# Kernel optimization log

Measured on AMD Instinct MI355X. Metric: run time of the kernel, lower is better.

Reference implementation:

```python
import jax, jax.numpy as jnp
import numpy as np

B, H, N, M, C = 64, 8, 16384, 64, 1024
IVH = 3 * M + 6  # per-head interface size: k(M), beta, g, s(3), gamma, e(M), a(M)


def setup_inputs() -> dict:
    key = jax.random.key(0)
    k1, k2, k3, k4 = jax.random.split(key, 4)
    return {
        "x": jax.random.normal(k1, (B, C), dtype=jnp.float32),
        "current_memory": jax.random.normal(k2, (B, N, M), dtype=jnp.float32),
        "w_prev": jax.random.uniform(k3, (B, H, N), dtype=jnp.float32),
        "W": jax.random.normal(k4, (C, H * IVH), dtype=jnp.float32) * (1.0 / np.sqrt(C)),
        "b": jnp.zeros((H * IVH,), dtype=jnp.float32),
    }


def reference(x, current_memory, w_prev, W, b):
    eps = 1e-16
    iv = (x @ W + b).reshape(B, H, IVH)
    k = iv[..., :M]                                   # [B,H,M] content key
    beta = jax.nn.softplus(iv[..., M])                # [B,H] key strength
    g = jax.nn.sigmoid(iv[..., M + 1])                # [B,H] interpolation gate
    s = jax.nn.softmax(iv[..., M + 2:M + 5], axis=-1) # [B,H,3] shift weights
    gamma = 1.0 + jax.nn.softplus(iv[..., M + 5])     # [B,H] sharpening
    e = jax.nn.sigmoid(iv[..., M + 6:2 * M + 6])      # [B,H,M] erase
    a = iv[..., 2 * M + 6:3 * M + 6]                  # [B,H,M] add

    # content addressing: cosine similarity of k against every memory row
    num = jnp.einsum('bhm,bnm->bhn', k, current_memory)
    den = (jnp.linalg.norm(k, axis=-1)[..., None]
           * jnp.linalg.norm(current_memory, axis=-1)[:, None, :] + eps)
    cos = num / den                                   # [B,H,N]
    wc = jax.nn.softmax(beta[..., None] * cos, axis=-1)

    # gated interpolation with previous weighting
    wg = g[..., None] * wc + (1.0 - g[..., None]) * w_prev

    # circular conv1d shift with 3-tap kernel (shifts -1, 0, +1)
    ws = (s[..., 0:1] * jnp.roll(wg, 1, axis=-1)
          + s[..., 1:2] * wg
          + s[..., 2:3] * jnp.roll(wg, -1, axis=-1))

    # sharpening (power normalize)
    wp = ws ** gamma[..., None]
    w = wp / (jnp.sum(wp, axis=-1, keepdims=True) + eps)

    # read
    read_data = jnp.einsum('bhn,bnm->bhm', w, current_memory)
    return (read_data, w, e, a)
```

## Files before the change

kernel.cpp:

```cpp
#include <hip/hip_runtime.h>
#include <cstdint>
#include <cstddef>

#define B_    64
#define H_    8
#define N_    16384
#define M_    64
#define C_    1024
#define IVH_  198
#define J_    1584
#define NCHUNK_ 64

__device__ __forceinline__ float softplus_f(float x) {
    return (x > 20.f) ? x : log1pf(__expf(x));
}
__device__ __forceinline__ float sigmoid_f(float x) {
    return 1.f / (1.f + __expf(-x));
}

__global__ __launch_bounds__(64) void k_gemm(const float* __restrict__ x,
                                             const float* __restrict__ W,
                                             float* __restrict__ iv) {
    int lane = threadIdx.x;
    int j = blockIdx.x * 64 + lane;
    bool valid = (j < J_);
    int b0 = blockIdx.y * 16;
    int c0 = blockIdx.z * 128;
    const float* xb = x + (size_t)b0 * C_;
    float acc[16];
    #pragma unroll
    for (int i = 0; i < 16; ++i) acc[i] = 0.f;
    #pragma unroll 2
    for (int c = c0; c < c0 + 128; ++c) {
        float wv = valid ? W[(size_t)c * J_ + j] : 0.f;
        #pragma unroll
        for (int bi = 0; bi < 16; ++bi)
            acc[bi] = fmaf(xb[(size_t)bi * C_ + c], wv, acc[bi]);
    }
    if (valid) {
        #pragma unroll
        for (int bi = 0; bi < 16; ++bi)
            atomicAdd(&iv[(size_t)(b0 + bi) * J_ + j], acc[bi]);
    }
}

__global__ void k_params(const float* __restrict__ iv, const float* __restrict__ bias,
                         float* __restrict__ kbuf, float* __restrict__ P,
                         float* __restrict__ out_e, float* __restrict__ out_a) {
    int bh = blockIdx.x;
    int m  = threadIdx.x;
    int b = bh >> 3, h = bh & 7;
    const float* row = iv + (size_t)b * J_ + h * IVH_;
    const float* bb  = bias + h * IVH_;
    float kv = row[m] + bb[m];
    kbuf[(size_t)bh * 64 + m] = kv;
    float s = kv * kv;
    #pragma unroll
    for (int o = 32; o > 0; o >>= 1) s += __shfl_down(s, o, 64);
    float ev = row[70 + m] + bb[70 + m];
    out_e[(size_t)bh * 64 + m] = sigmoid_f(ev);
    out_a[(size_t)bh * 64 + m] = row[134 + m] + bb[134 + m];
    if (m == 0) {
        float knorm = sqrtf(s);
        float v0 = row[64] + bb[64];
        float v1 = row[65] + bb[65];
        float v2 = row[66] + bb[66];
        float v3 = row[67] + bb[67];
        float v4 = row[68] + bb[68];
        float v5 = row[69] + bb[69];
        float beta = softplus_f(v0);
        float g = sigmoid_f(v1);
        float mx = fmaxf(v2, fmaxf(v3, v4));
        float e2 = __expf(v2 - mx), e3 = __expf(v3 - mx), e4 = __expf(v4 - mx);
        float inv = 1.f / (e2 + e3 + e4);
        float gamma = 1.f + softplus_f(v5);
        float* p = P + (size_t)bh * 8;
        p[0] = knorm; p[1] = beta; p[2] = g;
        p[3] = e2 * inv; p[4] = e3 * inv; p[5] = e4 * inv;
        p[6] = gamma;
    }
}

__global__ __launch_bounds__(256, 4) void k_passA(
        const float* __restrict__ mem, const float* __restrict__ kbuf,
        const float* __restrict__ P, float* __restrict__ z,
        float* __restrict__ pmax, float* __restrict__ psum) {
    __shared__ float zl[8 * 257];
    int t = threadIdx.x;
    int b = blockIdx.y;
    int n0 = blockIdx.x << 8;
    int w = t >> 6, lane = t & 63, sub = lane >> 4, mq = lane & 15;

    float4 kreg[8];
    #pragma unroll
    for (int h = 0; h < 8; ++h)
        kreg[h] = *(const float4*)(kbuf + (((size_t)b * 8 + h) << 6) + mq * 4);
    float beta = 0.f, knorm = 1.f;
    if (mq < 8) {
        const float* p = P + (((size_t)b * 8 + mq) << 3);
        knorm = p[0]; beta = p[1];
    }
    const float* mb = mem + ((size_t)b * N_ + n0) * M_;

    #pragma unroll
    for (int rr = 0; rr < 16; ++rr) {
        int row = (w << 6) + (rr << 2) + sub;
        float4 mv = *(const float4*)(mb + (size_t)row * M_ + mq * 4);
        float pr[9];
        #pragma unroll
        for (int h = 0; h < 8; ++h)
            pr[h] = kreg[h].x * mv.x + kreg[h].y * mv.y
                  + kreg[h].z * mv.z + kreg[h].w * mv.w;
        pr[8] = mv.x * mv.x + mv.y * mv.y + mv.z * mv.z + mv.w * mv.w;
        #pragma unroll
        for (int o = 1; o < 16; o <<= 1) {
            #pragma unroll
            for (int i = 0; i < 9; ++i) pr[i] += __shfl_xor(pr[i], o, 64);
        }
        if (mq < 8) {
            float rn = sqrtf(pr[8]);
            zl[mq * 257 + row] = beta * pr[mq] / (knorm * rn + 1e-16f);
        }
    }
    __syncthreads();

    #pragma unroll
    for (int h = 0; h < 8; ++h)
        z[(((size_t)b * 8 + h) << 14) + n0 + t] = zl[h * 257 + t];

    #pragma unroll
    for (int q = 0; q < 2; ++q) {
        int h = w * 2 + q;
        float a0 = zl[h * 257 + lane],       a1 = zl[h * 257 + lane + 64];
        float a2 = zl[h * 257 + lane + 128], a3 = zl[h * 257 + lane + 192];
        float mx = fmaxf(fmaxf(a0, a1), fmaxf(a2, a3));
        #pragma unroll
        for (int o = 32; o > 0; o >>= 1) mx = fmaxf(mx, __shfl_down(mx, o, 64));
        mx = __shfl(mx, 0, 64);
        float se = __expf(a0 - mx) + __expf(a1 - mx) + __expf(a2 - mx) + __expf(a3 - mx);
        #pragma unroll
        for (int o = 32; o > 0; o >>= 1) se += __shfl_down(se, o, 64);
        if (lane == 0) {
            pmax[(((size_t)b * 8 + h) << 6) + blockIdx.x] = mx;
            psum[(((size_t)b * 8 + h) << 6) + blockIdx.x] = se;
        }
    }
}

__global__ void k_stats(const float* __restrict__ pmax, const float* __restrict__ psum,
                        float* __restrict__ stats) {
    int bh = blockIdx.x * 4 + (threadIdx.x >> 6);
    int lane = threadIdx.x & 63;
    float m = pmax[((size_t)bh << 6) + lane];
    float s = psum[((size_t)bh << 6) + lane];
    float mx = m;
    #pragma unroll
    for (int o = 32; o > 0; o >>= 1) mx = fmaxf(mx, __shfl_down(mx, o, 64));
    mx = __shfl(mx, 0, 64);
    float sc = s * __expf(m - mx);
    #pragma unroll
    for (int o = 32; o > 0; o >>= 1) sc += __shfl_down(sc, o, 64);
    if (lane == 0) { stats[bh * 2] = mx; stats[bh * 2 + 1] = 1.f / sc; }
}

__global__ __launch_bounds__(256, 4) void k_passB(
        const float* __restrict__ mem, const float* __restrict__ z,
        const float* __restrict__ wprev, const float* __restrict__ P,
        const float* __restrict__ stats, float* __restrict__ out_w,
        float* __restrict__ sumwp, float* __restrict__ readAcc) {
    __shared__ float smem[3072 + 2064 + 32];
    float* wp_s  = smem;
    float* wgl   = smem + 3072;
    float* racc2 = smem + 3072;
    float* sums  = smem + 3072 + 2064;

    int t = threadIdx.x;
    int b = blockIdx.y;
    int n0 = blockIdx.x << 8;
    int n = n0 + t;
    int w = t >> 6, lane = t & 63, sub = lane >> 4, mq = lane & 15;

    #pragma unroll
    for (int h = 0; h < 8; ++h) {
        size_t bh = (size_t)b * 8 + h;
        float Mx = stats[bh * 2], iS = stats[bh * 2 + 1];
        float g = P[bh * 8 + 2];
        float wc = __expf(z[(bh << 14) + n] - Mx) * iS;
        wgl[h * 258 + t + 1] = fmaf(g, wc, (1.f - g) * wprev[(bh << 14) + n]);
    }
    if (t < 2) {
        int nh   = (t == 0) ? ((n0 + N_ - 1) & (N_ - 1)) : ((n0 + 256) & (N_ - 1));
        int slot = (t == 0) ? 0 : 257;
        #pragma unroll
        for (int h = 0; h < 8; ++h) {
            size_t bh = (size_t)b * 8 + h;
            float Mx = stats[bh * 2], iS = stats[bh * 2 + 1];
            float g = P[bh * 8 + 2];
            float wc = __expf(z[(bh << 14) + nh] - Mx) * iS;
            wgl[h * 258 + slot] = fmaf(g, wc, (1.f - g) * wprev[(bh << 14) + nh]);
        }
    }
    __syncthreads();

    float wpv[8];
    #pragma unroll
    for (int h = 0; h < 8; ++h) {
        size_t bh = (size_t)b * 8 + h;
        float s0 = P[bh * 8 + 3], s1 = P[bh * 8 + 4], s2 = P[bh * 8 + 5];
        float gam = P[bh * 8 + 6];
        float wsv = s0 * wgl[h * 258 + t] + s1 * wgl[h * 258 + t + 1]
                  + s2 * wgl[h * 258 + t + 2];
        float v = __powf(wsv, gam);
        wpv[h] = v;
        out_w[(bh << 14) + n] = v;
    }
    #pragma unroll
    for (int h = 0; h < 8; ++h) {
        float s = wpv[h];
        #pragma unroll
        for (int o = 32; o > 0; o >>= 1) s += __shfl_down(s, o, 64);
        if (lane == 0) sums[w * 8 + h] = s;
    }
    *(float4*)(wp_s + t * 12)     = make_float4(wpv[0], wpv[1], wpv[2], wpv[3]);
    *(float4*)(wp_s + t * 12 + 4) = make_float4(wpv[4], wpv[5], wpv[6], wpv[7]);
    __syncthreads();
    if (t < 8)
        atomicAdd(&sumwp[b * 8 + t], sums[t] + sums[8 + t] + sums[16 + t] + sums[24 + t]);

    float4 acc[8];
    #pragma unroll
    for (int h = 0; h < 8; ++h) acc[h] = make_float4(0.f, 0.f, 0.f, 0.f);
    const float* mb = mem + ((size_t)b * N_ + n0) * M_;
    #pragma unroll
    for (int rr = 0; rr < 16; ++rr) {
        int row = (w << 6) + (rr << 2) + sub;
        float4 mv = *(const float4*)(mb + (size_t)row * M_ + mq * 4);
        float4 wA = *(const float4*)(wp_s + row * 12);
        float4 wB = *(const float4*)(wp_s + row * 12 + 4);
        float wv8[8] = {wA.x, wA.y, wA.z, wA.w, wB.x, wB.y, wB.z, wB.w};
        #pragma unroll
        for (int h = 0; h < 8; ++h) {
            acc[h].x = fmaf(wv8[h], mv.x, acc[h].x);
            acc[h].y = fmaf(wv8[h], mv.y, acc[h].y);
            acc[h].z = fmaf(wv8[h], mv.z, acc[h].z);
            acc[h].w = fmaf(wv8[h], mv.w, acc[h].w);
        }
    }
    #pragma unroll
    for (int h = 0; h < 8; ++h) {
        #pragma unroll
        for (int o = 32; o >= 16; o >>= 1) {
            acc[h].x += __shfl_down(acc[h].x, o, 64);
            acc[h].y += __shfl_down(acc[h].y, o, 64);
            acc[h].z += __shfl_down(acc[h].z, o, 64);
            acc[h].w += __shfl_down(acc[h].w, o, 64);
        }
    }
    if (lane < 16) {
        #pragma unroll
        for (int h = 0; h < 8; ++h)
            *(float4*)(racc2 + ((w * 8 + h) << 6) + mq * 4) = acc[h];
    }
    __syncthreads();
    #pragma unroll
    for (int r = 0; r < 2; ++r) {
        int idx = r * 256 + t;
        float s = racc2[idx] + racc2[512 + idx] + racc2[1024 + idx] + racc2[1536 + idx];
        atomicAdd(&readAcc[(size_t)b * 512 + idx], s);
    }
}

__global__ void k_norm(float* __restrict__ out_w, const float* __restrict__ sumwp) {
    size_t idx = (size_t)blockIdx.x * 256 + threadIdx.x;
    int bh = (int)((idx * 4) >> 14);
    float inv = 1.f / (sumwp[bh] + 1e-16f);
    float4* p = (float4*)out_w + idx;
    float4 v = *p;
    v.x *= inv; v.y *= inv; v.z *= inv; v.w *= inv;
    *p = v;
}

__global__ void k_read(const float* __restrict__ readAcc, const float* __restrict__ sumwp,
                       float* __restrict__ out_rd) {
    int i = blockIdx.x * 256 + threadIdx.x;
    int bh = i >> 6;
    out_rd[i] = readAcc[i] / (sumwp[bh] + 1e-16f);
}

extern "C" void kernel_launch(void* const* d_in, const int* in_sizes, int n_in,
                              void* d_out, int out_size, void* d_ws, size_t ws_size,
                              hipStream_t stream) {
    const float* x     = (const float*)d_in[0];
    const float* mem   = (const float*)d_in[1];
    const float* wprev = (const float*)d_in[2];
    const float* W     = (const float*)d_in[3];
    const float* bias  = (const float*)d_in[4];

    float* out   = (float*)d_out;
    float* out_rd = out;
    float* out_w  = out + 32768;
    float* out_e  = out + 32768 + 8388608;
    float* out_a  = out_e + 32768;

    float* ws     = (float*)d_ws;
    float* iv      = ws;
    float* kbuf    = iv + 101376;
    float* P       = kbuf + 32768;
    float* zbuf    = P + 4096;
    float* pmax    = zbuf + 8388608;
    float* psum    = pmax + 32768;
    float* stats   = psum + 32768;
    float* sumwp   = stats + 1024;
    float* readAcc = sumwp + 512;

    hipMemsetAsync(iv, 0, (size_t)101376 * 4, stream);
    hipMemsetAsync(sumwp, 0, (size_t)(512 + 32768) * 4, stream);

    k_gemm  <<<dim3(25, 4, 8), 64, 0, stream>>>(x, W, iv);
    k_params<<<512, 64, 0, stream>>>(iv, bias, kbuf, P, out_e, out_a);
    k_passA <<<dim3(NCHUNK_, B_), 256, 0, stream>>>(mem, kbuf, P, zbuf, pmax, psum);
    k_stats <<<128, 256, 0, stream>>>(pmax, psum, stats);
    k_passB <<<dim3(NCHUNK_, B_), 256, 0, stream>>>(mem, zbuf, wprev, P, stats,
                                                    out_w, sumwp, readAcc);
    k_norm  <<<8192, 256, 0, stream>>>(out_w, sumwp);
    k_read  <<<128, 256, 0, stream>>>(readAcc, sumwp, out_rd);
}
```

Baseline: 538.1 us.

## Fuse params and stats kernels into passes, use DPP reductions, reverse passB order

Removes the separate k_params, k_stats and k_read launches. Parameter derivation moves into passA/passB, the softmax-stat merge into passB, and the e/a/read outputs into a single finish kernel. passA folds beta/knorm into the key and replaces shuffle-xor reductions with DPP row ops. passB walks chunks in reverse so it can reuse memory rows still cached from passA, the GEMM split-K is doubled, and the two memsets are merged into one. Each passB block recomputes the per-head stats redundantly, and the k-norm is recomputed in every passA block.

```diff
diff --git a/kernel.cpp b/kernel.cpp
--- a/kernel.cpp
+++ b/kernel.cpp
@@ -18,6 +18,24 @@
     return 1.f / (1.f + __expf(-x));
 }
 
+template<int CTRL>
+__device__ __forceinline__ float dppf(float x) {
+    return __int_as_float(__builtin_amdgcn_update_dpp(
+        0, __float_as_int(x), CTRL, 0xF, 0xF, true));
+}
+#define RED16(v) { v += dppf<0xB1>(v); v += dppf<0x4E>(v); \
+                   v += dppf<0x128>(v); v += dppf<0x124>(v); }
+
+__device__ __forceinline__ float sel8(const float p[8], int i) {
+    float r01 = (i & 1) ? p[1] : p[0];
+    float r23 = (i & 1) ? p[3] : p[2];
+    float r45 = (i & 1) ? p[5] : p[4];
+    float r67 = (i & 1) ? p[7] : p[6];
+    float a = (i & 2) ? r23 : r01;
+    float c = (i & 2) ? r67 : r45;
+    return (i & 4) ? c : a;
+}
+
 __global__ __launch_bounds__(64) void k_gemm(const float* __restrict__ x,
                                              const float* __restrict__ W,
                                              float* __restrict__ iv) {
@@ -25,13 +43,13 @@
     int j = blockIdx.x * 64 + lane;
     bool valid = (j < J_);
     int b0 = blockIdx.y * 16;
-    int c0 = blockIdx.z * 128;
+    int c0 = blockIdx.z * 64;
     const float* xb = x + (size_t)b0 * C_;
     float acc[16];
     #pragma unroll
     for (int i = 0; i < 16; ++i) acc[i] = 0.f;
-    #pragma unroll 2
-    for (int c = c0; c < c0 + 128; ++c) {
+    #pragma unroll 8
+    for (int c = c0; c < c0 + 64; ++c) {
         float wv = valid ? W[(size_t)c * J_ + j] : 0.f;
         #pragma unroll
         for (int bi = 0; bi < 16; ++bi)
@@ -44,46 +62,9 @@
     }
 }
 
-__global__ void k_params(const float* __restrict__ iv, const float* __restrict__ bias,
-                         float* __restrict__ kbuf, float* __restrict__ P,
-                         float* __restrict__ out_e, float* __restrict__ out_a) {
-    int bh = blockIdx.x;
-    int m  = threadIdx.x;
-    int b = bh >> 3, h = bh & 7;
-    const float* row = iv + (size_t)b * J_ + h * IVH_;
-    const float* bb  = bias + h * IVH_;
-    float kv = row[m] + bb[m];
-    kbuf[(size_t)bh * 64 + m] = kv;
-    float s = kv * kv;
-    #pragma unroll
-    for (int o = 32; o > 0; o >>= 1) s += __shfl_down(s, o, 64);
-    float ev = row[70 + m] + bb[70 + m];
-    out_e[(size_t)bh * 64 + m] = sigmoid_f(ev);
-    out_a[(size_t)bh * 64 + m] = row[134 + m] + bb[134 + m];
-    if (m == 0) {
-        float knorm = sqrtf(s);
-        float v0 = row[64] + bb[64];
-        float v1 = row[65] + bb[65];
-        float v2 = row[66] + bb[66];
-        float v3 = row[67] + bb[67];
-        float v4 = row[68] + bb[68];
-        float v5 = row[69] + bb[69];
-        float beta = softplus_f(v0);
-        float g = sigmoid_f(v1);
-        float mx = fmaxf(v2, fmaxf(v3, v4));
-        float e2 = __expf(v2 - mx), e3 = __expf(v3 - mx), e4 = __expf(v4 - mx);
-        float inv = 1.f / (e2 + e3 + e4);
-        float gamma = 1.f + softplus_f(v5);
-        float* p = P + (size_t)bh * 8;
-        p[0] = knorm; p[1] = beta; p[2] = g;
-        p[3] = e2 * inv; p[4] = e3 * inv; p[5] = e4 * inv;
-        p[6] = gamma;
-    }
-}
-
 __global__ __launch_bounds__(256, 4) void k_passA(
-        const float* __restrict__ mem, const float* __restrict__ kbuf,
-        const float* __restrict__ P, float* __restrict__ z,
+        const float* __restrict__ mem, const float* __restrict__ iv,
+        const float* __restrict__ bias, float* __restrict__ z,
         float* __restrict__ pmax, float* __restrict__ psum) {
     __shared__ float zl[8 * 257];
     int t = threadIdx.x;
@@ -91,17 +72,34 @@
     int n0 = blockIdx.x << 8;
     int w = t >> 6, lane = t & 63, sub = lane >> 4, mq = lane & 15;
 
+    const float* ivb = iv + (size_t)b * J_;
     float4 kreg[8];
-    #pragma unroll
-    for (int h = 0; h < 8; ++h)
-        kreg[h] = *(const float4*)(kbuf + (((size_t)b * 8 + h) << 6) + mq * 4);
-    float beta = 0.f, knorm = 1.f;
-    if (mq < 8) {
-        const float* p = P + (((size_t)b * 8 + mq) << 3);
-        knorm = p[0]; beta = p[1];
-    }
+    float nq[8];
+    #pragma unroll
+    for (int h = 0; h < 8; ++h) {
+        const float* ivh = ivb + h * IVH_;
+        const float* bbh = bias + h * IVH_;
+        float2 a0 = *(const float2*)(ivh + mq * 4);
+        float2 a1 = *(const float2*)(ivh + mq * 4 + 2);
+        float2 c0 = *(const float2*)(bbh + mq * 4);
+        float2 c1 = *(const float2*)(bbh + mq * 4 + 2);
+        float4 kv = make_float4(a0.x + c0.x, a0.y + c0.y, a1.x + c1.x, a1.y + c1.y);
+        float q = kv.x * kv.x + kv.y * kv.y + kv.z * kv.z + kv.w * kv.w;
+        RED16(q);
+        nq[h] = q;
+        kreg[h] = kv;
+    }
+    float kn[8];
+    #pragma unroll
+    for (int h = 0; h < 8; ++h) {
+        kn[h] = sqrtf(nq[h]);
+        float v0 = ivb[h * IVH_ + 64] + bias[h * IVH_ + 64];
+        float s = softplus_f(v0) / kn[h];
+        kreg[h].x *= s; kreg[h].y *= s; kreg[h].z *= s; kreg[h].w *= s;
+    }
+    float epsl = 1e-16f / sel8(kn, mq & 7);
+
     const float* mb = mem + ((size_t)b * N_ + n0) * M_;
-
     #pragma unroll
     for (int rr = 0; rr < 16; ++rr) {
         int row = (w << 6) + (rr << 2) + sub;
@@ -113,13 +111,10 @@
                   + kreg[h].z * mv.z + kreg[h].w * mv.w;
         pr[8] = mv.x * mv.x + mv.y * mv.y + mv.z * mv.z + mv.w * mv.w;
         #pragma unroll
-        for (int o = 1; o < 16; o <<= 1) {
-            #pragma unroll
-            for (int i = 0; i < 9; ++i) pr[i] += __shfl_xor(pr[i], o, 64);
-        }
+        for (int i = 0; i < 9; ++i) { float vv = pr[i]; RED16(vv); pr[i] = vv; }
         if (mq < 8) {
             float rn = sqrtf(pr[8]);
-            zl[mq * 257 + row] = beta * pr[mq] / (knorm * rn + 1e-16f);
+            zl[mq * 257 + row] = sel8(pr, mq) / (rn + epsl);
         }
     }
     __syncthreads();
@@ -147,44 +142,64 @@
     }
 }
 
-__global__ void k_stats(const float* __restrict__ pmax, const float* __restrict__ psum,
-                        float* __restrict__ stats) {
-    int bh = blockIdx.x * 4 + (threadIdx.x >> 6);
-    int lane = threadIdx.x & 63;
-    float m = pmax[((size_t)bh << 6) + lane];
-    float s = psum[((size_t)bh << 6) + lane];
-    float mx = m;
-    #pragma unroll
-    for (int o = 32; o > 0; o >>= 1) mx = fmaxf(mx, __shfl_down(mx, o, 64));
-    mx = __shfl(mx, 0, 64);
-    float sc = s * __expf(m - mx);
-    #pragma unroll
-    for (int o = 32; o > 0; o >>= 1) sc += __shfl_down(sc, o, 64);
-    if (lane == 0) { stats[bh * 2] = mx; stats[bh * 2 + 1] = 1.f / sc; }
-}
-
 __global__ __launch_bounds__(256, 4) void k_passB(
         const float* __restrict__ mem, const float* __restrict__ z,
-        const float* __restrict__ wprev, const float* __restrict__ P,
-        const float* __restrict__ stats, float* __restrict__ out_w,
+        const float* __restrict__ wprev, const float* __restrict__ iv,
+        const float* __restrict__ bias, const float* __restrict__ pmax,
+        const float* __restrict__ psum, float* __restrict__ out_w,
         float* __restrict__ sumwp, float* __restrict__ readAcc) {
     __shared__ float smem[3072 + 2064 + 32];
+    __shared__ float pl[64];
     float* wp_s  = smem;
     float* wgl   = smem + 3072;
     float* racc2 = smem + 3072;
     float* sums  = smem + 3072 + 2064;
 
     int t = threadIdx.x;
-    int b = blockIdx.y;
-    int n0 = blockIdx.x << 8;
+    int b  = (B_ - 1) - blockIdx.y;
+    int ck = (NCHUNK_ - 1) - blockIdx.x;
+    int n0 = ck << 8;
     int n = n0 + t;
     int w = t >> 6, lane = t & 63, sub = lane >> 4, mq = lane & 15;
 
     #pragma unroll
-    for (int h = 0; h < 8; ++h) {
+    for (int q = 0; q < 2; ++q) {
+        int h = w * 2 + q;
         size_t bh = (size_t)b * 8 + h;
-        float Mx = stats[bh * 2], iS = stats[bh * 2 + 1];
-        float g = P[bh * 8 + 2];
+        float m = pmax[(bh << 6) + lane];
+        float s = psum[(bh << 6) + lane];
+        float mx = m;
+        #pragma unroll
+        for (int o = 32; o > 0; o >>= 1) mx = fmaxf(mx, __shfl_xor(mx, o, 64));
+        float sc = s * __expf(m - mx);
+        #pragma unroll
+        for (int o = 32; o > 0; o >>= 1) sc += __shfl_xor(sc, o, 64);
+        if (lane == 0) { pl[h * 8 + 0] = mx; pl[h * 8 + 1] = 1.f / sc; }
+    }
+    if (t < 8) {
+        const float* ivh = iv + (size_t)b * J_ + t * IVH_;
+        const float* bbh = bias + t * IVH_;
+        float v1 = ivh[65] + bbh[65];
+        float v2 = ivh[66] + bbh[66];
+        float v3 = ivh[67] + bbh[67];
+        float v4 = ivh[68] + bbh[68];
+        float v5 = ivh[69] + bbh[69];
+        float mx3 = fmaxf(v2, fmaxf(v3, v4));
+        float e2 = __expf(v2 - mx3), e3 = __expf(v3 - mx3), e4 = __expf(v4 - mx3);
+        float inv = 1.f / (e2 + e3 + e4);
+        pl[t * 8 + 2] = sigmoid_f(v1);
+        pl[t * 8 + 3] = e2 * inv;
+        pl[t * 8 + 4] = e3 * inv;
+        pl[t * 8 + 5] = e4 * inv;
+        pl[t * 8 + 6] = 1.f + softplus_f(v5);
+    }
+    __syncthreads();
+
+    #pragma unroll
+    for (int h = 0; h < 8; ++h) {
+        size_t bh = (size_t)b * 8 + h;
+        float Mx = pl[h * 8 + 0], iS = pl[h * 8 + 1];
+        float g = pl[h * 8 + 2];
         float wc = __expf(z[(bh << 14) + n] - Mx) * iS;
         wgl[h * 258 + t + 1] = fmaf(g, wc, (1.f - g) * wprev[(bh << 14) + n]);
     }
@@ -194,8 +209,8 @@
         #pragma unroll
         for (int h = 0; h < 8; ++h) {
             size_t bh = (size_t)b * 8 + h;
-            float Mx = stats[bh * 2], iS = stats[bh * 2 + 1];
-            float g = P[bh * 8 + 2];
+            float Mx = pl[h * 8 + 0], iS = pl[h * 8 + 1];
+            float g = pl[h * 8 + 2];
             float wc = __expf(z[(bh << 14) + nh] - Mx) * iS;
             wgl[h * 258 + slot] = fmaf(g, wc, (1.f - g) * wprev[(bh << 14) + nh]);
         }
@@ -206,8 +221,8 @@
     #pragma unroll
     for (int h = 0; h < 8; ++h) {
         size_t bh = (size_t)b * 8 + h;
-        float s0 = P[bh * 8 + 3], s1 = P[bh * 8 + 4], s2 = P[bh * 8 + 5];
-        float gam = P[bh * 8 + 6];
+        float s0 = pl[h * 8 + 3], s1 = pl[h * 8 + 4], s2 = pl[h * 8 + 5];
+        float gam = pl[h * 8 + 6];
         float wsv = s0 * wgl[h * 258 + t] + s1 * wgl[h * 258 + t + 1]
                   + s2 * wgl[h * 258 + t + 2];
         float v = __powf(wsv, gam);
@@ -270,21 +285,32 @@
     }
 }
 
-__global__ void k_norm(float* __restrict__ out_w, const float* __restrict__ sumwp) {
-    size_t idx = (size_t)blockIdx.x * 256 + threadIdx.x;
-    int bh = (int)((idx * 4) >> 14);
+__global__ void k_finish(float* __restrict__ out_w, const float* __restrict__ sumwp,
+                         const float* __restrict__ readAcc, const float* __restrict__ iv,
+                         const float* __restrict__ bias, float* __restrict__ out_rd,
+                         float* __restrict__ out_e, float* __restrict__ out_a) {
+    int t = threadIdx.x;
+    size_t idx = (size_t)blockIdx.x * 256 + t;
+    int bh = (int)(idx >> 12);
     float inv = 1.f / (sumwp[bh] + 1e-16f);
     float4* p = (float4*)out_w + idx;
     float4 v = *p;
     v.x *= inv; v.y *= inv; v.z *= inv; v.w *= inv;
     *p = v;
-}
-
-__global__ void k_read(const float* __restrict__ readAcc, const float* __restrict__ sumwp,
-                       float* __restrict__ out_rd) {
-    int i = blockIdx.x * 256 + threadIdx.x;
-    int bh = i >> 6;
-    out_rd[i] = readAcc[i] / (sumwp[bh] + 1e-16f);
+    if (blockIdx.x < 128) {
+        int i = blockIdx.x * 256 + t;
+        out_rd[i] = readAcc[i] / (sumwp[i >> 6] + 1e-16f);
+    } else if (blockIdx.x < 256) {
+        int i = (blockIdx.x - 128) * 256 + t;
+        int bb = i >> 9, h = (i >> 6) & 7, m = i & 63;
+        int off = h * IVH_ + 70 + m;
+        out_e[i] = sigmoid_f(iv[(size_t)bb * J_ + off] + bias[off]);
+    } else if (blockIdx.x < 384) {
+        int i = (blockIdx.x - 256) * 256 + t;
+        int bb = i >> 9, h = (i >> 6) & 7, m = i & 63;
+        int off = h * IVH_ + 134 + m;
+        out_a[i] = iv[(size_t)bb * J_ + off] + bias[off];
+    }
 }
 
 extern "C" void kernel_launch(void* const* d_in, const int* in_sizes, int n_in,
@@ -302,26 +328,20 @@
     float* out_e  = out + 32768 + 8388608;
     float* out_a  = out_e + 32768;
 
-    float* ws     = (float*)d_ws;
+    float* ws      = (float*)d_ws;
     float* iv      = ws;
-    float* kbuf    = iv + 101376;
-    float* P       = kbuf + 32768;
-    float* zbuf    = P + 4096;
+    float* sumwp   = iv + 101376;
+    float* readAcc = sumwp + 512;
+    float* zbuf    = readAcc + 32768;
     float* pmax    = zbuf + 8388608;
     float* psum    = pmax + 32768;
-    float* stats   = psum + 32768;
-    float* sumwp   = stats + 1024;
-    float* readAcc = sumwp + 512;
-
-    hipMemsetAsync(iv, 0, (size_t)101376 * 4, stream);
-    hipMemsetAsync(sumwp, 0, (size_t)(512 + 32768) * 4, stream);
-
-    k_gemm  <<<dim3(25, 4, 8), 64, 0, stream>>>(x, W, iv);
-    k_params<<<512, 64, 0, stream>>>(iv, bias, kbuf, P, out_e, out_a);
-    k_passA <<<dim3(NCHUNK_, B_), 256, 0, stream>>>(mem, kbuf, P, zbuf, pmax, psum);
-    k_stats <<<128, 256, 0, stream>>>(pmax, psum, stats);
-    k_passB <<<dim3(NCHUNK_, B_), 256, 0, stream>>>(mem, zbuf, wprev, P, stats,
-                                                    out_w, sumwp, readAcc);
-    k_norm  <<<8192, 256, 0, stream>>>(out_w, sumwp);
-    k_read  <<<128, 256, 0, stream>>>(readAcc, sumwp, out_rd);
-}
+
+    hipMemsetAsync(iv, 0, (size_t)(101376 + 512 + 32768) * 4, stream);
+
+    k_gemm  <<<dim3(25, 4, 16), 64, 0, stream>>>(x, W, iv);
+    k_passA <<<dim3(NCHUNK_, B_), 256, 0, stream>>>(mem, iv, bias, zbuf, pmax, psum);
+    k_passB <<<dim3(NCHUNK_, B_), 256, 0, stream>>>(mem, zbuf, wprev, iv, bias,
+                                                    pmax, psum, out_w, sumwp, readAcc);
+    k_finish<<<8192, 256, 0, stream>>>(out_w, sumwp, readAcc, iv, bias,
+                                       out_rd, out_e, out_a);
+}
```

After: 570.9 us. 6.1% more time.

## Fold beta/knorm into key, fuse stats into passB, merge final kernels and memsets

Applied to the files above, without the earlier changes.

Pre-scales the key by beta/||k|| in the params kernel so pass A divides only by the row norm plus a scaled epsilon. Pass A now gives each row 8 lanes of 8 elements, cutting the shuffle-reduction steps, and all lanes write via a select. The global softmax stats reduction moves into pass B, which caches per-head parameters in shared memory, removing the k_stats launch. The normalize and read kernels merge into one, and the two memsets merge into one. The cost is redundant stats reduction in every pass-B block.

```diff
diff --git a/kernel.cpp b/kernel.cpp
--- a/kernel.cpp
+++ b/kernel.cpp
@@ -16,6 +16,15 @@
 }
 __device__ __forceinline__ float sigmoid_f(float x) {
     return 1.f / (1.f + __expf(-x));
+}
+__device__ __forceinline__ float sel8(const float p[8], int i) {
+    float r01 = (i & 1) ? p[1] : p[0];
+    float r23 = (i & 1) ? p[3] : p[2];
+    float r45 = (i & 1) ? p[5] : p[4];
+    float r67 = (i & 1) ? p[7] : p[6];
+    float a = (i & 2) ? r23 : r01;
+    float c = (i & 2) ? r67 : r45;
+    return (i & 4) ? c : a;
 }
 
 __global__ __launch_bounds__(64) void k_gemm(const float* __restrict__ x,
@@ -53,138 +62,146 @@
     const float* row = iv + (size_t)b * J_ + h * IVH_;
     const float* bb  = bias + h * IVH_;
     float kv = row[m] + bb[m];
-    kbuf[(size_t)bh * 64 + m] = kv;
     float s = kv * kv;
     #pragma unroll
-    for (int o = 32; o > 0; o >>= 1) s += __shfl_down(s, o, 64);
+    for (int o = 32; o > 0; o >>= 1) s += __shfl_xor(s, o, 64);
+    float kn = sqrtf(s);
+    float beta = softplus_f(row[64] + bb[64]);
+    kbuf[(size_t)bh * 64 + m] = kv * (beta / kn);
     float ev = row[70 + m] + bb[70 + m];
     out_e[(size_t)bh * 64 + m] = sigmoid_f(ev);
     out_a[(size_t)bh * 64 + m] = row[134 + m] + bb[134 + m];
     if (m == 0) {
-        float knorm = sqrtf(s);
-        float v0 = row[64] + bb[64];
         float v1 = row[65] + bb[65];
         float v2 = row[66] + bb[66];
         float v3 = row[67] + bb[67];
         float v4 = row[68] + bb[68];
         float v5 = row[69] + bb[69];
-        float beta = softplus_f(v0);
-        float g = sigmoid_f(v1);
-        float mx = fmaxf(v2, fmaxf(v3, v4));
-        float e2 = __expf(v2 - mx), e3 = __expf(v3 - mx), e4 = __expf(v4 - mx);
+        float mx3 = fmaxf(v2, fmaxf(v3, v4));
+        float e2 = __expf(v2 - mx3), e3 = __expf(v3 - mx3), e4 = __expf(v4 - mx3);
         float inv = 1.f / (e2 + e3 + e4);
-        float gamma = 1.f + softplus_f(v5);
         float* p = P + (size_t)bh * 8;
-        p[0] = knorm; p[1] = beta; p[2] = g;
-        p[3] = e2 * inv; p[4] = e3 * inv; p[5] = e4 * inv;
-        p[6] = gamma;
-    }
-}
-
-__global__ __launch_bounds__(256, 4) void k_passA(
+        p[0] = 1e-16f / kn;
+        p[1] = sigmoid_f(v1);
+        p[2] = e2 * inv; p[3] = e3 * inv; p[4] = e4 * inv;
+        p[5] = 1.f + softplus_f(v5);
+    }
+}
+
+__global__ __launch_bounds__(256, 4) void k_A(
         const float* __restrict__ mem, const float* __restrict__ kbuf,
         const float* __restrict__ P, float* __restrict__ z,
         float* __restrict__ pmax, float* __restrict__ psum) {
-    __shared__ float zl[8 * 257];
+    __shared__ float zl[8 * 264];
     int t = threadIdx.x;
     int b = blockIdx.y;
-    int n0 = blockIdx.x << 8;
-    int w = t >> 6, lane = t & 63, sub = lane >> 4, mq = lane & 15;
-
-    float4 kreg[8];
-    #pragma unroll
-    for (int h = 0; h < 8; ++h)
-        kreg[h] = *(const float4*)(kbuf + (((size_t)b * 8 + h) << 6) + mq * 4);
-    float beta = 0.f, knorm = 1.f;
-    if (mq < 8) {
-        const float* p = P + (((size_t)b * 8 + mq) << 3);
-        knorm = p[0]; beta = p[1];
-    }
+    int ck = blockIdx.x;
+    int n0 = ck << 8;
+    int w = t >> 6, lane = t & 63, sub8 = lane >> 3, mq8 = lane & 7;
+
+    float4 ka[8], kb[8];
+    #pragma unroll
+    for (int h = 0; h < 8; ++h) {
+        const float* kr = kbuf + (((size_t)b * 8 + h) << 6) + mq8 * 8;
+        ka[h] = *(const float4*)(kr);
+        kb[h] = *(const float4*)(kr + 4);
+    }
+    float epsl = P[(((size_t)b * 8 + mq8) << 3)];
+
     const float* mb = mem + ((size_t)b * N_ + n0) * M_;
-
-    #pragma unroll
-    for (int rr = 0; rr < 16; ++rr) {
-        int row = (w << 6) + (rr << 2) + sub;
-        float4 mv = *(const float4*)(mb + (size_t)row * M_ + mq * 4);
+    #pragma unroll 2
+    for (int rr = 0; rr < 8; ++rr) {
+        int row = (w << 6) + (rr << 3) + sub8;
+        const float* mr = mb + (size_t)row * M_ + mq8 * 8;
+        float4 m0 = *(const float4*)(mr);
+        float4 m1 = *(const float4*)(mr + 4);
         float pr[9];
         #pragma unroll
         for (int h = 0; h < 8; ++h)
-            pr[h] = kreg[h].x * mv.x + kreg[h].y * mv.y
-                  + kreg[h].z * mv.z + kreg[h].w * mv.w;
-        pr[8] = mv.x * mv.x + mv.y * mv.y + mv.z * mv.z + mv.w * mv.w;
-        #pragma unroll
-        for (int o = 1; o < 16; o <<= 1) {
+            pr[h] = ka[h].x*m0.x + ka[h].y*m0.y + ka[h].z*m0.z + ka[h].w*m0.w
+                  + kb[h].x*m1.x + kb[h].y*m1.y + kb[h].z*m1.z + kb[h].w*m1.w;
+        pr[8] = m0.x*m0.x+m0.y*m0.y+m0.z*m0.z+m0.w*m0.w
+              + m1.x*m1.x+m1.y*m1.y+m1.z*m1.z+m1.w*m1.w;
+        #pragma unroll
+        for (int o = 1; o < 8; o <<= 1) {
             #pragma unroll
             for (int i = 0; i < 9; ++i) pr[i] += __shfl_xor(pr[i], o, 64);
         }
-        if (mq < 8) {
-            float rn = sqrtf(pr[8]);
-            zl[mq * 257 + row] = beta * pr[mq] / (knorm * rn + 1e-16f);
-        }
+        float rn = sqrtf(pr[8]);
+        zl[mq8 * 264 + row] = sel8(pr, mq8) / (rn + epsl);
     }
     __syncthreads();
 
     #pragma unroll
     for (int h = 0; h < 8; ++h)
-        z[(((size_t)b * 8 + h) << 14) + n0 + t] = zl[h * 257 + t];
-
-    #pragma unroll
-    for (int q = 0; q < 2; ++q) {
-        int h = w * 2 + q;
-        float a0 = zl[h * 257 + lane],       a1 = zl[h * 257 + lane + 64];
-        float a2 = zl[h * 257 + lane + 128], a3 = zl[h * 257 + lane + 192];
+        z[(((size_t)b * 8 + h) << 14) + n0 + t] = zl[h * 264 + t];
+
+    #pragma unroll
+    for (int q2 = 0; q2 < 2; ++q2) {
+        int h = w * 2 + q2;
+        float a0 = zl[h * 264 + lane],       a1 = zl[h * 264 + lane + 64];
+        float a2 = zl[h * 264 + lane + 128], a3 = zl[h * 264 + lane + 192];
         float mx = fmaxf(fmaxf(a0, a1), fmaxf(a2, a3));
         #pragma unroll
-        for (int o = 32; o > 0; o >>= 1) mx = fmaxf(mx, __shfl_down(mx, o, 64));
-        mx = __shfl(mx, 0, 64);
+        for (int o = 32; o > 0; o >>= 1) mx = fmaxf(mx, __shfl_xor(mx, o, 64));
         float se = __expf(a0 - mx) + __expf(a1 - mx) + __expf(a2 - mx) + __expf(a3 - mx);
         #pragma unroll
-        for (int o = 32; o > 0; o >>= 1) se += __shfl_down(se, o, 64);
+        for (int o = 32; o > 0; o >>= 1) se += __shfl_xor(se, o, 64);
         if (lane == 0) {
-            pmax[(((size_t)b * 8 + h) << 6) + blockIdx.x] = mx;
-            psum[(((size_t)b * 8 + h) << 6) + blockIdx.x] = se;
-        }
-    }
-}
-
-__global__ void k_stats(const float* __restrict__ pmax, const float* __restrict__ psum,
-                        float* __restrict__ stats) {
-    int bh = blockIdx.x * 4 + (threadIdx.x >> 6);
-    int lane = threadIdx.x & 63;
-    float m = pmax[((size_t)bh << 6) + lane];
-    float s = psum[((size_t)bh << 6) + lane];
-    float mx = m;
-    #pragma unroll
-    for (int o = 32; o > 0; o >>= 1) mx = fmaxf(mx, __shfl_down(mx, o, 64));
-    mx = __shfl(mx, 0, 64);
-    float sc = s * __expf(m - mx);
-    #pragma unroll
-    for (int o = 32; o > 0; o >>= 1) sc += __shfl_down(sc, o, 64);
-    if (lane == 0) { stats[bh * 2] = mx; stats[bh * 2 + 1] = 1.f / sc; }
-}
-
-__global__ __launch_bounds__(256, 4) void k_passB(
+            pmax[(((size_t)b * 8 + h) << 6) + ck] = mx;
+            psum[(((size_t)b * 8 + h) << 6) + ck] = se;
+        }
+    }
+}
+
+__global__ __launch_bounds__(256, 4) void k_B(
         const float* __restrict__ mem, const float* __restrict__ z,
         const float* __restrict__ wprev, const float* __restrict__ P,
-        const float* __restrict__ stats, float* __restrict__ out_w,
-        float* __restrict__ sumwp, float* __restrict__ readAcc) {
-    __shared__ float smem[3072 + 2064 + 32];
+        const float* __restrict__ pmax, const float* __restrict__ psum,
+        float* __restrict__ out_w, float* __restrict__ sumwp,
+        float* __restrict__ readAcc) {
+    __shared__ float smem[3072 + 2064 + 32 + 64];
     float* wp_s  = smem;
     float* wgl   = smem + 3072;
     float* racc2 = smem + 3072;
-    float* sums  = smem + 3072 + 2064;
+    float* sums  = smem + 5136;
+    float* pl    = smem + 5168;
 
     int t = threadIdx.x;
-    int b = blockIdx.y;
-    int n0 = blockIdx.x << 8;
+    int b  = blockIdx.y;
+    int ck = blockIdx.x;
+    int n0 = ck << 8;
     int n = n0 + t;
     int w = t >> 6, lane = t & 63, sub = lane >> 4, mq = lane & 15;
 
     #pragma unroll
-    for (int h = 0; h < 8; ++h) {
+    for (int q2 = 0; q2 < 2; ++q2) {
+        int h = w * 2 + q2;
         size_t bh = (size_t)b * 8 + h;
-        float Mx = stats[bh * 2], iS = stats[bh * 2 + 1];
-        float g = P[bh * 8 + 2];
+        float m = pmax[(bh << 6) + lane];
+        float s = psum[(bh << 6) + lane];
+        float mx = m;
+        #pragma unroll
+        for (int o = 32; o > 0; o >>= 1) mx = fmaxf(mx, __shfl_xor(mx, o, 64));
+        float sc = s * __expf(m - mx);
+        #pragma unroll
+        for (int o = 32; o > 0; o >>= 1) sc += __shfl_xor(sc, o, 64);
+        if (lane == 0) { pl[h * 8 + 0] = mx; pl[h * 8 + 1] = 1.f / sc; }
+    }
+    if (t < 8) {
+        const float* p = P + (((size_t)b * 8 + t) << 3);
+        pl[t * 8 + 2] = p[1];
+        pl[t * 8 + 3] = p[2];
+        pl[t * 8 + 4] = p[3];
+        pl[t * 8 + 5] = p[4];
+        pl[t * 8 + 6] = p[5];
+    }
+    __syncthreads();
+
+    #pragma unroll
+    for (int h = 0; h < 8; ++h) {
+        size_t bh = (size_t)b * 8 + h;
+        float Mx = pl[h * 8 + 0], iS = pl[h * 8 + 1], g = pl[h * 8 + 2];
         float wc = __expf(z[(bh << 14) + n] - Mx) * iS;
         wgl[h * 258 + t + 1] = fmaf(g, wc, (1.f - g) * wprev[(bh << 14) + n]);
     }
@@ -194,8 +211,7 @@
         #pragma unroll
         for (int h = 0; h < 8; ++h) {
             size_t bh = (size_t)b * 8 + h;
-            float Mx = stats[bh * 2], iS = stats[bh * 2 + 1];
-            float g = P[bh * 8 + 2];
+            float Mx = pl[h * 8 + 0], iS = pl[h * 8 + 1], g = pl[h * 8 + 2];
             float wc = __expf(z[(bh << 14) + nh] - Mx) * iS;
             wgl[h * 258 + slot] = fmaf(g, wc, (1.f - g) * wprev[(bh << 14) + nh]);
         }
@@ -206,8 +222,8 @@
     #pragma unroll
     for (int h = 0; h < 8; ++h) {
         size_t bh = (size_t)b * 8 + h;
-        float s0 = P[bh * 8 + 3], s1 = P[bh * 8 + 4], s2 = P[bh * 8 + 5];
-        float gam = P[bh * 8 + 6];
+        float s0 = pl[h * 8 + 3], s1 = pl[h * 8 + 4], s2 = pl[h * 8 + 5];
+        float gam = pl[h * 8 + 6];
         float wsv = s0 * wgl[h * 258 + t] + s1 * wgl[h * 258 + t + 1]
                   + s2 * wgl[h * 258 + t + 2];
         float v = __powf(wsv, gam);
@@ -224,8 +240,6 @@
     *(float4*)(wp_s + t * 12)     = make_float4(wpv[0], wpv[1], wpv[2], wpv[3]);
     *(float4*)(wp_s + t * 12 + 4) = make_float4(wpv[4], wpv[5], wpv[6], wpv[7]);
     __syncthreads();
-    if (t < 8)
-        atomicAdd(&sumwp[b * 8 + t], sums[t] + sums[8 + t] + sums[16 + t] + sums[24 + t]);
 
     float4 acc[8];
     #pragma unroll
@@ -262,6 +276,8 @@
             *(float4*)(racc2 + ((w * 8 + h) << 6) + mq * 4) = acc[h];
     }
     __syncthreads();
+    if (t < 8)
+        atomicAdd(&sumwp[b * 8 + t], sums[t] + sums[8 + t] + sums[16 + t] + sums[24 + t]);
     #pragma unroll
     for (int r = 0; r < 2; ++r) {
         int idx = r * 256 + t;
@@ -270,21 +286,20 @@
     }
 }
 
-__global__ void k_norm(float* __restrict__ out_w, const float* __restrict__ sumwp) {
-    size_t idx = (size_t)blockIdx.x * 256 + threadIdx.x;
-    int bh = (int)((idx * 4) >> 14);
+__global__ void k_F(float* __restrict__ out_w, const float* __restrict__ sumwp,
+                    const float* __restrict__ readAcc, float* __restrict__ out_rd) {
+    int t = threadIdx.x;
+    size_t idx = (size_t)blockIdx.x * 256 + t;
+    int bh = (int)(idx >> 12);
     float inv = 1.f / (sumwp[bh] + 1e-16f);
     float4* p = (float4*)out_w + idx;
     float4 v = *p;
     v.x *= inv; v.y *= inv; v.z *= inv; v.w *= inv;
     *p = v;
-}
-
-__global__ void k_read(const float* __restrict__ readAcc, const float* __restrict__ sumwp,
-                       float* __restrict__ out_rd) {
-    int i = blockIdx.x * 256 + threadIdx.x;
-    int bh = i >> 6;
-    out_rd[i] = readAcc[i] / (sumwp[bh] + 1e-16f);
+    if (blockIdx.x < 128) {
+        int i = blockIdx.x * 256 + t;
+        out_rd[i] = readAcc[i] / (sumwp[i >> 6] + 1e-16f);
+    }
 }
 
 extern "C" void kernel_launch(void* const* d_in, const int* in_sizes, int n_in,
@@ -296,32 +311,28 @@
     const float* W     = (const float*)d_in[3];
     const float* bias  = (const float*)d_in[4];
 
-    float* out   = (float*)d_out;
+    float* out    = (float*)d_out;
     float* out_rd = out;
     float* out_w  = out + 32768;
     float* out_e  = out + 32768 + 8388608;
     float* out_a  = out_e + 32768;
 
-    float* ws     = (float*)d_ws;
+    float* ws      = (float*)d_ws;
     float* iv      = ws;
-    float* kbuf    = iv + 101376;
+    float* sumwp   = iv + 101376;
+    float* readAcc = sumwp + 512;
+    float* kbuf    = readAcc + 32768;
     float* P       = kbuf + 32768;
     float* zbuf    = P + 4096;
     float* pmax    = zbuf + 8388608;
     float* psum    = pmax + 32768;
-    float* stats   = psum + 32768;
-    float* sumwp   = stats + 1024;
-    float* readAcc = sumwp + 512;
-
-    hipMemsetAsync(iv, 0, (size_t)101376 * 4, stream);
-    hipMemsetAsync(sumwp, 0, (size_t)(512 + 32768) * 4, stream);
+
+    hipMemsetAsync(iv, 0, (size_t)(101376 + 512 + 32768) * 4, stream);
 
     k_gemm  <<<dim3(25, 4, 8), 64, 0, stream>>>(x, W, iv);
     k_params<<<512, 64, 0, stream>>>(iv, bias, kbuf, P, out_e, out_a);
-    k_passA <<<dim3(NCHUNK_, B_), 256, 0, stream>>>(mem, kbuf, P, zbuf, pmax, psum);
-    k_stats <<<128, 256, 0, stream>>>(pmax, psum, stats);
-    k_passB <<<dim3(NCHUNK_, B_), 256, 0, stream>>>(mem, zbuf, wprev, P, stats,
+    k_A     <<<dim3(NCHUNK_, B_), 256, 0, stream>>>(mem, kbuf, P, zbuf, pmax, psum);
+    k_B     <<<dim3(NCHUNK_, B_), 256, 0, stream>>>(mem, zbuf, wprev, P, pmax, psum,
                                                     out_w, sumwp, readAcc);
-    k_norm  <<<8192, 256, 0, stream>>>(out_w, sumwp);
-    k_read  <<<128, 256, 0, stream>>>(readAcc, sumwp, out_rd);
-}
+    k_F     <<<8192, 256, 0, stream>>>(out_w, sumwp, readAcc, out_rd);
+}
```

Measured after the change: 543.5 us. No clear change (+1.0%).
